# Optimization experiments

Measured on AMD Instinct MI355X. Metric: run time of the kernel, lower is better.

Reference implementation:

```python
import jax, jax.numpy as jnp
import numpy as np

TIME_PENALTY = 0.01
PONDER_EPS = 0.01
TIME_LIMIT = 16
BATCH, INPUT_SIZE, HIDDEN_SIZE = 4096, 1024, 1024


def setup_inputs() -> dict:
    key = jax.random.key(0)
    ks = jax.random.split(key, 8)
    s_in = 1.0 / np.sqrt(INPUT_SIZE + 1)
    s_h = 1.0 / np.sqrt(HIDDEN_SIZE)
    return {
        "inputs": jax.random.normal(ks[0], (BATCH, INPUT_SIZE), jnp.float32),
        "hidden": jax.random.normal(ks[1], (BATCH, HIDDEN_SIZE), jnp.float32),
        # RNNCell params (input size = INPUT_SIZE + 1 for the first-step flag)
        "W_ih": jax.random.uniform(ks[2], (HIDDEN_SIZE, INPUT_SIZE + 1), jnp.float32, -s_in, s_in),
        "b_ih": jax.random.uniform(ks[3], (HIDDEN_SIZE,), jnp.float32, -s_in, s_in),
        "W_hh": jax.random.uniform(ks[4], (HIDDEN_SIZE, HIDDEN_SIZE), jnp.float32, -s_h, s_h),
        "b_hh": jax.random.uniform(ks[5], (HIDDEN_SIZE,), jnp.float32, -s_h, s_h),
        # halting unit: Linear(hidden_size, 1), bias initialized to -1.0
        "W_halt": jax.random.uniform(ks[6], (1, HIDDEN_SIZE), jnp.float32, -s_h, s_h),
        "b_halt": jnp.full((1,), -1.0, jnp.float32),
    }


def _act_forward(inputs, hidden, W_ih, b_ih, W_hh, b_hh, W_halt, b_halt):
    B = inputs.shape[0]
    H = W_hh.shape[0]
    dt = inputs.dtype
    budget = jnp.asarray(1.0 - PONDER_EPS, dt)
    # input projection: the last input column is the first-step flag, so
    # step_inputs @ W_ih^T == inputs @ W_ih[:, :-1]^T + flag * W_ih[:, -1]
    x_base = inputs @ W_ih[:, :-1].T + b_ih  # (B, H)
    flag_col = W_ih[:, -1]                    # (H,)
    flags = (jnp.arange(TIME_LIMIT - 1) == 0).astype(dt)

    def step(carry, flag):
        h, halt_accum, cont, tot_h, tot_rem, tot_steps = carry
        h = jnp.tanh(x_base + flag * flag_col + h @ W_hh.T + b_hh)  # (B, H)
        step_halt = jax.nn.sigmoid(h @ W_halt.T + b_halt)           # (B, 1)
        masked_halt = jnp.where(cont, step_halt, 0.0)
        # halt accumulator is detached in the original (torch.no_grad)
        halt_accum = halt_accum + jax.lax.stop_gradient(masked_halt)
        ending = cont & (halt_accum + step_halt > budget)
        cont = cont & (~ending)
        tot_steps = tot_steps + cont.astype(dt)
        masked_rem = jnp.where(ending, 1.0 - halt_accum, 0.0)
        combined = masked_halt + masked_rem
        tot_h = tot_h + combined * h
        tot_rem = tot_rem + masked_halt
        return (h, halt_accum, cont, tot_h, tot_rem, tot_steps), None

    init = (
        hidden,
        jnp.zeros((B, 1), dt),
        jnp.ones((B, 1), bool),
        jnp.zeros((B, H), dt),
        jnp.zeros((B, 1), dt),
        jnp.zeros((B, 1), dt),
    )
    (h, halt_accum, cont, tot_h, tot_rem, tot_steps), _ = jax.lax.scan(step, init, flags)
    # for-else branch: elements still continuing after the loop get the remainder
    # (zero-contribution if everything halted early, matching the early break)
    tot_h = tot_h + jnp.where(cont, 1.0 - halt_accum, 0.0) * h
    ponder_cost = -TIME_PENALTY * tot_rem.mean()
    return tot_h, ponder_cost, tot_steps + 1.0


def reference(inputs, hidden, W_ih, b_ih, W_hh, b_hh, W_halt, b_halt):
    return _act_forward(inputs, hidden, W_ih, b_ih, W_hh, b_hh, W_halt, b_halt)
```

## Files before the change

kernel.cpp:

```cpp
#include <hip/hip_runtime.h>
#include <math.h>

#define BATCH 4096
#define HID   1024
#define KDIM  1024
#define NSTEP 15
#define KV    3072
#define NCHUNK (KV / 64)

#define TMM 128
#define TNN 64
#define LDAH 72

typedef _Float16 half8 __attribute__((ext_vector_type(8)));
typedef float floatx4 __attribute__((ext_vector_type(4)));

__device__ __forceinline__ _Float16 f16hi(float x) { return (_Float16)x; }

__global__ __launch_bounds__(256) void setup_kernel(
    const float* __restrict__ W_ih, const float* __restrict__ W_hh,
    const float* __restrict__ inputs, const float* __restrict__ hidden,
    _Float16* __restrict__ B3ih, _Float16* __restrict__ B3hh,
    _Float16* __restrict__ Ihi, _Float16* __restrict__ Ilo,
    _Float16* __restrict__ Hhi, _Float16* __restrict__ Hlo,
    float* __restrict__ flagcol, int* __restrict__ list0, int* __restrict__ counts,
    float* __restrict__ halt_accum, float* __restrict__ tot_rem) {
    size_t idx = (size_t)blockIdx.x * 256 + threadIdx.x;
    {
        float x = inputs[idx];
        _Float16 h = f16hi(x);
        Ihi[idx] = h; Ilo[idx] = (_Float16)(x - (float)h);
        float y = hidden[idx];
        _Float16 g = f16hi(y);
        Hhi[idx] = g; Hlo[idx] = (_Float16)(y - (float)g);
    }
    if (idx < (size_t)KDIM * KDIM) {
        int n = (int)(idx >> 10), k = (int)(idx & 1023);
        float w = W_hh[idx];
        _Float16 hi = f16hi(w);
        _Float16 lo = (_Float16)(w - (float)hi);
        size_t base = (size_t)n * KV;
        B3hh[base + k] = hi; B3hh[base + 1024 + k] = lo; B3hh[base + 2048 + k] = hi;
        float w2 = W_ih[(size_t)n * 1025 + k];
        _Float16 hi2 = f16hi(w2);
        _Float16 lo2 = (_Float16)(w2 - (float)hi2);
        B3ih[base + k] = hi2; B3ih[base + 1024 + k] = lo2; B3ih[base + 2048 + k] = hi2;
    }
    if (idx < BATCH) { list0[idx] = idx; halt_accum[idx] = 0.f; tot_rem[idx] = 0.f; }
    if (idx < KDIM) flagcol[idx] = W_ih[idx * 1025 + 1024];
    if (idx < 16) counts[idx] = (idx == 0) ? BATCH : 0;
}

__global__ __launch_bounds__(256) void mfma_step_kernel(
    const _Float16* __restrict__ Ahi, const _Float16* __restrict__ Alo,
    const _Float16* __restrict__ B3, const float* __restrict__ bias,
    const float* __restrict__ xbase, const float* __restrict__ flagcol, float flag,
    const int* __restrict__ list, const int* __restrict__ pcount,
    float* __restrict__ hout, _Float16* __restrict__ houthi, _Float16* __restrict__ houtlo,
    float* __restrict__ xout, int mode) {
    int count = pcount ? *pcount : BATCH;
    int row0 = blockIdx.x * TMM;
    if (row0 >= count) return;
    int col0 = blockIdx.y * TNN;

    __shared__ _Float16 Asm[2][TMM][LDAH];
    __shared__ _Float16 Bsm[2][TNN][LDAH];

    int t = threadIdx.x;
    int lane = t & 63, w = t >> 6;
    int wm = (w & 1) * 64, wn = (w >> 1) * 32;

    int arw[4], aq8[4]; size_t aoff[4];
#pragma unroll
    for (int l = 0; l < 4; l++) {
        int q = t + l * 256;
        int r = q >> 3, qk = q & 7;
        arw[l] = r; aq8[l] = qk * 8;
        int rr = row0 + r;
        int g = (rr < count) ? (list ? list[rr] : rr) : 0;
        aoff[l] = (size_t)g * KDIM + qk * 8;
    }
    int brw[2], bq8[2]; size_t boff[2];
#pragma unroll
    for (int l = 0; l < 2; l++) {
        int q = t + l * 256;
        int r = q >> 3, qk = q & 7;
        brw[l] = r; bq8[l] = qk * 8;
        boff[l] = (size_t)(col0 + r) * KV + qk * 8;
    }

    floatx4 acc[4][2];
#pragma unroll
    for (int i = 0; i < 4; i++)
#pragma unroll
        for (int j = 0; j < 2; j++) acc[i][j] = (floatx4)(0.f);

    int l15 = lane & 15, l4 = lane >> 4;

    half8 av[4], bv[2];
#pragma unroll
    for (int l = 0; l < 4; l++) av[l] = *(const half8*)(Ahi + aoff[l]);
#pragma unroll
    for (int l = 0; l < 2; l++) bv[l] = *(const half8*)(B3 + boff[l]);
#pragma unroll
    for (int l = 0; l < 4; l++) *(half8*)(&Asm[0][arw[l]][aq8[l]]) = av[l];
#pragma unroll
    for (int l = 0; l < 2; l++) *(half8*)(&Bsm[0][brw[l]][bq8[l]]) = bv[l];
    __syncthreads();

    int p = 0;
    for (int it = 0; it < NCHUNK; it++) {
        if (it + 1 < NCHUNK) {
            int k0v = (it + 1) << 6;
            const _Float16* Asrc = (k0v < 2048) ? Ahi : Alo;
            int kp = k0v & 1023;
#pragma unroll
            for (int l = 0; l < 4; l++) av[l] = *(const half8*)(Asrc + aoff[l] + kp);
#pragma unroll
            for (int l = 0; l < 2; l++) bv[l] = *(const half8*)(B3 + boff[l] + k0v);
        }
#pragma unroll
        for (int ks = 0; ks < 2; ks++) {
            int ko = ks * 32 + l4 * 8;
            half8 af[4], bf[2];
#pragma unroll
            for (int fi = 0; fi < 4; fi++)
                af[fi] = *(const half8*)(&Asm[p][wm + fi * 16 + l15][ko]);
#pragma unroll
            for (int fj = 0; fj < 2; fj++)
                bf[fj] = *(const half8*)(&Bsm[p][wn + fj * 16 + l15][ko]);
#pragma unroll
            for (int fi = 0; fi < 4; fi++)
#pragma unroll
                for (int fj = 0; fj < 2; fj++)
                    acc[fi][fj] = __builtin_amdgcn_mfma_f32_16x16x32_f16(
                        af[fi], bf[fj], acc[fi][fj], 0, 0, 0);
        }
        if (it + 1 < NCHUNK) {
            int q = p ^ 1;
#pragma unroll
            for (int l = 0; l < 4; l++) *(half8*)(&Asm[q][arw[l]][aq8[l]]) = av[l];
#pragma unroll
            for (int l = 0; l < 2; l++) *(half8*)(&Bsm[q][brw[l]][bq8[l]]) = bv[l];
        }
        __syncthreads();
        p ^= 1;
    }

#pragma unroll
    for (int fi = 0; fi < 4; fi++) {
#pragma unroll
        for (int rr = 0; rr < 4; rr++) {
            int lm = wm + fi * 16 + l4 * 4 + rr;
            int grd = row0 + lm;
            if (grd >= count) continue;
            int g = list ? list[grd] : grd;
#pragma unroll
            for (int fj = 0; fj < 2; fj++) {
                int c = col0 + wn + fj * 16 + l15;
                float v = acc[fi][fj][rr];
                if (mode == 0) {
                    xout[(size_t)g * KDIM + c] = v + bias[c];
                } else {
                    v += xbase[(size_t)g * KDIM + c] + flag * flagcol[c] + bias[c];
                    v = tanhf(v);
                    hout[(size_t)g * KDIM + c] = v;
                    _Float16 hi = f16hi(v);
                    houthi[(size_t)g * KDIM + c] = hi;
                    houtlo[(size_t)g * KDIM + c] = (_Float16)(v - (float)hi);
                }
            }
        }
    }
}

__global__ __launch_bounds__(256) void halt_kernel(
    const float* __restrict__ h, const float* __restrict__ W_halt,
    const float* __restrict__ b_halt,
    const int* __restrict__ list, const int* __restrict__ pcount,
    int* __restrict__ list_next, int* __restrict__ pcount_next,
    float* __restrict__ halt_accum, float* __restrict__ tot_rem,
    float* __restrict__ tot_h, float* __restrict__ steps_out,
    int stepnum, int first) {
    int count = *pcount;
    int wid = threadIdx.x >> 6, lane = threadIdx.x & 63;
    int r = blockIdx.x * 4 + wid;
    if (r >= count) return;
    int row = list[r];
    const float* hr = h + (size_t)row * HID;

    float dot = 0.f;
#pragma unroll
    for (int q = 0; q < 4; q++) {
        int c = q * 256 + lane * 4;
        float4 hv = *(const float4*)(hr + c);
        float4 wv = *(const float4*)(W_halt + c);
        dot += hv.x * wv.x + hv.y * wv.y + hv.z * wv.z + hv.w * wv.w;
    }
#pragma unroll
    for (int off = 32; off > 0; off >>= 1) dot += __shfl_down(dot, off);

    float combined = 0.f;
    if (lane == 0) {
        float p = 1.f / (1.f + expf(-(dot + b_halt[0])));
        float S = halt_accum[row] + p;
        halt_accum[row] = S;
        tot_rem[row] += p;
        bool ending = (S + p) > 0.99f;
        if (ending) {
            combined = p + (1.f - S);
            steps_out[row] = (float)stepnum;
        } else {
            combined = p;
            int idx = atomicAdd(pcount_next, 1);
            list_next[idx] = row;
        }
    }
    combined = __shfl(combined, 0);

    float* th = tot_h + (size_t)row * HID;
#pragma unroll
    for (int q = 0; q < 4; q++) {
        int c = q * 256 + lane * 4;
        float4 hv = *(const float4*)(hr + c);
        float4 ov;
        if (first) {
            ov.x = combined * hv.x; ov.y = combined * hv.y;
            ov.z = combined * hv.z; ov.w = combined * hv.w;
        } else {
            ov = *(const float4*)(th + c);
            ov.x += combined * hv.x; ov.y += combined * hv.y;
            ov.z += combined * hv.z; ov.w += combined * hv.w;
        }
        *(float4*)(th + c) = ov;
    }
}

__global__ __launch_bounds__(256) void epilogue_kernel(
    const float* __restrict__ h, const int* __restrict__ list,
    const int* __restrict__ pcount, const float* __restrict__ halt_accum,
    const float* __restrict__ tot_rem,
    float* __restrict__ tot_h, float* __restrict__ steps_out,
    float* __restrict__ ponder) {
    if (blockIdx.x == 1024) {
        __shared__ float red[4];
        int t = threadIdx.x;
        float v = 0.f;
#pragma unroll
        for (int i = 0; i < 16; i++) v += tot_rem[t + i * 256];
#pragma unroll
        for (int off = 32; off > 0; off >>= 1) v += __shfl_down(v, off);
        int lane = t & 63, wid = t >> 6;
        if (lane == 0) red[wid] = v;
        __syncthreads();
        if (t == 0) ponder[0] = (red[0] + red[1] + red[2] + red[3]) * (-0.01f / 4096.f);
        return;
    }
    int count = *pcount;
    int wid = threadIdx.x >> 6, lane = threadIdx.x & 63;
    int r = blockIdx.x * 4 + wid;
    if (r >= count) return;
    int row = list[r];
    float cmb = 1.f - halt_accum[row];
    if (lane == 0) steps_out[row] = 16.f;
    const float* hr = h + (size_t)row * HID;
    float* th = tot_h + (size_t)row * HID;
#pragma unroll
    for (int q = 0; q < 4; q++) {
        int c = q * 256 + lane * 4;
        float4 hv = *(const float4*)(hr + c);
        float4 ov = *(const float4*)(th + c);
        ov.x += cmb * hv.x; ov.y += cmb * hv.y;
        ov.z += cmb * hv.z; ov.w += cmb * hv.w;
        *(float4*)(th + c) = ov;
    }
}

extern "C" void kernel_launch(void* const* d_in, const int* in_sizes, int n_in,
                              void* d_out, int out_size, void* d_ws, size_t ws_size,
                              hipStream_t stream) {
    const float* inputs = (const float*)d_in[0];
    const float* hidden = (const float*)d_in[1];
    const float* W_ih   = (const float*)d_in[2];
    const float* b_ih   = (const float*)d_in[3];
    const float* W_hh   = (const float*)d_in[4];
    const float* b_hh   = (const float*)d_in[5];
    const float* W_halt = (const float*)d_in[6];
    const float* b_halt = (const float*)d_in[7];
    float* out = (float*)d_out;

    float* ws = (float*)d_ws;
    const size_t NM = (size_t)BATCH * HID;
    float* xbase = ws;
    float* h     = xbase + NM;
    _Float16* B3ih = (_Float16*)(h + NM);
    _Float16* B3hh = B3ih + (size_t)HID * KV;
    _Float16* Ahi0 = B3hh + (size_t)HID * KV;
    _Float16* Alo0 = Ahi0 + NM;
    _Float16* Ahi1 = Alo0 + NM;
    _Float16* Alo1 = Ahi1 + NM;
    float* flagcol = (float*)(Alo1 + NM);
    float* halt_accum = flagcol + KDIM;
    float* tot_rem = halt_accum + BATCH;
    int* list0 = (int*)(tot_rem + BATCH);
    int* list1 = list0 + BATCH;
    int* counts = list1 + BATCH;

    _Float16* Ahi[2] = {Ahi0, Ahi1};
    _Float16* Alo[2] = {Alo0, Alo1};
    int* lists[2] = {list0, list1};

    float* tot_h = out;
    float* ponder = out + NM;
    float* steps_out = ponder + 1;

    setup_kernel<<<16384, 256, 0, stream>>>(W_ih, W_hh, inputs, hidden,
                                            B3ih, B3hh, Ahi1, Alo1, Ahi0, Alo0,
                                            flagcol, list0, counts, halt_accum, tot_rem);

    mfma_step_kernel<<<dim3(32, 16), 256, 0, stream>>>(
        Ahi1, Alo1, B3ih, b_ih, nullptr, nullptr, 0.f, nullptr, nullptr,
        nullptr, nullptr, nullptr, xbase, 0);

    for (int t = 0; t < NSTEP; t++) {
        mfma_step_kernel<<<dim3(32, 16), 256, 0, stream>>>(
            Ahi[t & 1], Alo[t & 1], B3hh, b_hh, xbase, flagcol,
            (t == 0) ? 1.f : 0.f, lists[t & 1], counts + t,
            h, Ahi[(t + 1) & 1], Alo[(t + 1) & 1], nullptr, 1);
        halt_kernel<<<1024, 256, 0, stream>>>(h, W_halt, b_halt,
                                              lists[t & 1], counts + t,
                                              lists[(t + 1) & 1], counts + t + 1,
                                              halt_accum, tot_rem, tot_h, steps_out,
                                              t + 1, (t == 0) ? 1 : 0);
    }
    epilogue_kernel<<<1025, 256, 0, stream>>>(h, lists[1], counts + 15,
                                              halt_accum, tot_rem, tot_h, steps_out, ponder);
}
```

Baseline: 736.6 us.

## Pre-swizzle weights into MFMA fragment layout and drop fp32 hidden buffer

```diff
diff --git a/kernel.cpp b/kernel.cpp
--- a/kernel.cpp
+++ b/kernel.cpp
@@ -7,15 +7,17 @@
 #define NSTEP 15
 #define KV    3072
 #define NCHUNK (KV / 64)
-
-#define TMM 128
-#define TNN 64
-#define LDAH 72
+#define NSEC  (KV / 16)
+#define NT    (HID / 32)
+
 
 typedef _Float16 half8 __attribute__((ext_vector_type(8)));
-typedef float floatx4 __attribute__((ext_vector_type(4)));
-
-__device__ __forceinline__ _Float16 f16hi(float x) { return (_Float16)x; }
+typedef float floatx16 __attribute__((ext_vector_type(16)));
+
+__device__ __forceinline__ size_t b3addr(int n, int kv) {
+    return ((size_t)((n >> 5) * NSEC + (kv >> 4))) * 512 +
+           (size_t)(((n & 31) + 32 * ((kv >> 3) & 1)) * 8 + (kv & 7));
+}
 
 __global__ __launch_bounds__(256) void setup_kernel(
     const float* __restrict__ W_ih, const float* __restrict__ W_hh,
@@ -28,84 +30,79 @@
     size_t idx = (size_t)blockIdx.x * 256 + threadIdx.x;
     {
         float x = inputs[idx];
-        _Float16 h = f16hi(x);
+        _Float16 h = (_Float16)x;
         Ihi[idx] = h; Ilo[idx] = (_Float16)(x - (float)h);
         float y = hidden[idx];
-        _Float16 g = f16hi(y);
+        _Float16 g = (_Float16)y;
         Hhi[idx] = g; Hlo[idx] = (_Float16)(y - (float)g);
     }
     if (idx < (size_t)KDIM * KDIM) {
         int n = (int)(idx >> 10), k = (int)(idx & 1023);
         float w = W_hh[idx];
-        _Float16 hi = f16hi(w);
+        _Float16 hi = (_Float16)w;
         _Float16 lo = (_Float16)(w - (float)hi);
-        size_t base = (size_t)n * KV;
-        B3hh[base + k] = hi; B3hh[base + 1024 + k] = lo; B3hh[base + 2048 + k] = hi;
+        B3hh[b3addr(n, k)] = hi;
+        B3hh[b3addr(n, 1024 + k)] = lo;
+        B3hh[b3addr(n, 2048 + k)] = hi;
         float w2 = W_ih[(size_t)n * 1025 + k];
-        _Float16 hi2 = f16hi(w2);
+        _Float16 hi2 = (_Float16)w2;
         _Float16 lo2 = (_Float16)(w2 - (float)hi2);
-        B3ih[base + k] = hi2; B3ih[base + 1024 + k] = lo2; B3ih[base + 2048 + k] = hi2;
+        B3ih[b3addr(n, k)] = hi2;
+        B3ih[b3addr(n, 1024 + k)] = lo2;
+        B3ih[b3addr(n, 2048 + k)] = hi2;
     }
     if (idx < BATCH) { list0[idx] = idx; halt_accum[idx] = 0.f; tot_rem[idx] = 0.f; }
     if (idx < KDIM) flagcol[idx] = W_ih[idx * 1025 + 1024];
     if (idx < 16) counts[idx] = (idx == 0) ? BATCH : 0;
 }
 
-__global__ __launch_bounds__(256) void mfma_step_kernel(
+__global__ __launch_bounds__(128) void mfma_step_kernel(
     const _Float16* __restrict__ Ahi, const _Float16* __restrict__ Alo,
-    const _Float16* __restrict__ B3, const float* __restrict__ bias,
+    const _Float16* __restrict__ B3f, const float* __restrict__ bias,
     const float* __restrict__ xbase, const float* __restrict__ flagcol, float flag,
     const int* __restrict__ list, const int* __restrict__ pcount,
-    float* __restrict__ hout, _Float16* __restrict__ houthi, _Float16* __restrict__ houtlo,
+    _Float16* __restrict__ houthi, _Float16* __restrict__ houtlo,
     float* __restrict__ xout, int mode) {
     int count = pcount ? *pcount : BATCH;
-    int row0 = blockIdx.x * TMM;
+    int row0 = blockIdx.x * 64;
     if (row0 >= count) return;
-    int col0 = blockIdx.y * TNN;
-
-    __shared__ _Float16 Asm[2][TMM][LDAH];
-    __shared__ _Float16 Bsm[2][TNN][LDAH];
+    int col0 = blockIdx.y * 128;
+
+    __shared__ _Float16 Asm[2][64 * 64];
 
     int t = threadIdx.x;
     int lane = t & 63, w = t >> 6;
-    int wm = (w & 1) * 64, wn = (w >> 1) * 32;
-
-    int arw[4], aq8[4]; size_t aoff[4];
+    int l31 = lane & 31, l5 = lane >> 5;
+
+    int asl[4]; size_t aoff[4];
 #pragma unroll
     for (int l = 0; l < 4; l++) {
-        int q = t + l * 256;
+        int q = t + l * 128;
         int r = q >> 3, qk = q & 7;
-        arw[l] = r; aq8[l] = qk * 8;
+        asl[l] = r * 64 + ((qk ^ (r & 7)) << 3);
         int rr = row0 + r;
         int g = (rr < count) ? (list ? list[rr] : rr) : 0;
-        aoff[l] = (size_t)g * KDIM + qk * 8;
-    }
-    int brw[2], bq8[2]; size_t boff[2];
-#pragma unroll
-    for (int l = 0; l < 2; l++) {
-        int q = t + l * 256;
-        int r = q >> 3, qk = q & 7;
-        brw[l] = r; bq8[l] = qk * 8;
-        boff[l] = (size_t)(col0 + r) * KV + qk * 8;
-    }
-
-    floatx4 acc[4][2];
-#pragma unroll
-    for (int i = 0; i < 4; i++)
-#pragma unroll
-        for (int j = 0; j < 2; j++) acc[i][j] = (floatx4)(0.f);
-
-    int l15 = lane & 15, l4 = lane >> 4;
-
-    half8 av[4], bv[2];
+        aoff[l] = (size_t)g * KDIM + (size_t)(qk << 3);
+    }
+
+    const half8* B8 = (const half8*)B3f;
+    int nt0 = (col0 >> 5) + w * 2;
+    const half8* Bp0 = B8 + (size_t)nt0 * NSEC * 64;
+    const half8* Bp1 = B8 + (size_t)(nt0 + 1) * NSEC * 64;
+
+    floatx16 acc[2][2];
+#pragma unroll
+    for (int i = 0; i < 2; i++)
+#pragma unroll
+        for (int j = 0; j < 2; j++)
+#pragma unroll
+            for (int r = 0; r < 16; r++) acc[i][j][r] = 0.f;
+
+    half8 av[4];
 #pragma unroll
     for (int l = 0; l < 4; l++) av[l] = *(const half8*)(Ahi + aoff[l]);
 #pragma unroll
-    for (int l = 0; l < 2; l++) bv[l] = *(const half8*)(B3 + boff[l]);
-#pragma unroll
-    for (int l = 0; l < 4; l++) *(half8*)(&Asm[0][arw[l]][aq8[l]]) = av[l];
-#pragma unroll
-    for (int l = 0; l < 2; l++) *(half8*)(&Bsm[0][brw[l]][bq8[l]]) = bv[l];
+    for (int l = 0; l < 4; l++) *(half8*)(&Asm[0][asl[l]]) = av[l];
     __syncthreads();
 
     int p = 0;
@@ -113,59 +110,51 @@
         if (it + 1 < NCHUNK) {
             int k0v = (it + 1) << 6;
             const _Float16* Asrc = (k0v < 2048) ? Ahi : Alo;
-            int kp = k0v & 1023;
+            size_t kp = (size_t)(k0v & 1023);
 #pragma unroll
             for (int l = 0; l < 4; l++) av[l] = *(const half8*)(Asrc + aoff[l] + kp);
-#pragma unroll
-            for (int l = 0; l < 2; l++) bv[l] = *(const half8*)(B3 + boff[l] + k0v);
-        }
-#pragma unroll
-        for (int ks = 0; ks < 2; ks++) {
-            int ko = ks * 32 + l4 * 8;
-            half8 af[4], bf[2];
-#pragma unroll
-            for (int fi = 0; fi < 4; fi++)
-                af[fi] = *(const half8*)(&Asm[p][wm + fi * 16 + l15][ko]);
-#pragma unroll
-            for (int fj = 0; fj < 2; fj++)
-                bf[fj] = *(const half8*)(&Bsm[p][wn + fj * 16 + l15][ko]);
-#pragma unroll
-            for (int fi = 0; fi < 4; fi++)
-#pragma unroll
-                for (int fj = 0; fj < 2; fj++)
-                    acc[fi][fj] = __builtin_amdgcn_mfma_f32_16x16x32_f16(
-                        af[fi], bf[fj], acc[fi][fj], 0, 0, 0);
+        }
+#pragma unroll
+        for (int s = 0; s < 4; s++) {
+            int sg = it * 4 + s;
+            int gl = s * 2 + l5;
+            int ga = (gl ^ (l31 & 7)) << 3;
+            half8 a0 = *(const half8*)(&Asm[p][l31 * 64 + ga]);
+            half8 a1 = *(const half8*)(&Asm[p][(32 + l31) * 64 + ga]);
+            half8 b0 = Bp0[(size_t)sg * 64 + lane];
+            half8 b1 = Bp1[(size_t)sg * 64 + lane];
+            acc[0][0] = __builtin_amdgcn_mfma_f32_32x32x16_f16(a0, b0, acc[0][0], 0, 0, 0);
+            acc[0][1] = __builtin_amdgcn_mfma_f32_32x32x16_f16(a0, b1, acc[0][1], 0, 0, 0);
+            acc[1][0] = __builtin_amdgcn_mfma_f32_32x32x16_f16(a1, b0, acc[1][0], 0, 0, 0);
+            acc[1][1] = __builtin_amdgcn_mfma_f32_32x32x16_f16(a1, b1, acc[1][1], 0, 0, 0);
         }
         if (it + 1 < NCHUNK) {
             int q = p ^ 1;
 #pragma unroll
-            for (int l = 0; l < 4; l++) *(half8*)(&Asm[q][arw[l]][aq8[l]]) = av[l];
-#pragma unroll
-            for (int l = 0; l < 2; l++) *(half8*)(&Bsm[q][brw[l]][bq8[l]]) = bv[l];
+            for (int l = 0; l < 4; l++) *(half8*)(&Asm[q][asl[l]]) = av[l];
         }
         __syncthreads();
         p ^= 1;
     }
 
 #pragma unroll
-    for (int fi = 0; fi < 4; fi++) {
-#pragma unroll
-        for (int rr = 0; rr < 4; rr++) {
-            int lm = wm + fi * 16 + l4 * 4 + rr;
-            int grd = row0 + lm;
+    for (int fi = 0; fi < 2; fi++) {
+#pragma unroll
+        for (int r = 0; r < 16; r++) {
+            int rowid = (r & 3) + 8 * (r >> 2) + 4 * l5;
+            int grd = row0 + fi * 32 + rowid;
             if (grd >= count) continue;
             int g = list ? list[grd] : grd;
 #pragma unroll
             for (int fj = 0; fj < 2; fj++) {
-                int c = col0 + wn + fj * 16 + l15;
-                float v = acc[fi][fj][rr];
+                int c = col0 + w * 64 + fj * 32 + l31;
+                float v = acc[fi][fj][r];
                 if (mode == 0) {
                     xout[(size_t)g * KDIM + c] = v + bias[c];
                 } else {
                     v += xbase[(size_t)g * KDIM + c] + flag * flagcol[c] + bias[c];
                     v = tanhf(v);
-                    hout[(size_t)g * KDIM + c] = v;
-                    _Float16 hi = f16hi(v);
+                    _Float16 hi = (_Float16)v;
                     houthi[(size_t)g * KDIM + c] = hi;
                     houtlo[(size_t)g * KDIM + c] = (_Float16)(v - (float)hi);
                 }
@@ -175,8 +164,8 @@
 }
 
 __global__ __launch_bounds__(256) void halt_kernel(
-    const float* __restrict__ h, const float* __restrict__ W_halt,
-    const float* __restrict__ b_halt,
+    const _Float16* __restrict__ Hhi, const _Float16* __restrict__ Hlo,
+    const float* __restrict__ W_halt, const float* __restrict__ b_halt,
     const int* __restrict__ list, const int* __restrict__ pcount,
     int* __restrict__ list_next, int* __restrict__ pcount_next,
     float* __restrict__ halt_accum, float* __restrict__ tot_rem,
@@ -187,15 +176,22 @@
     int r = blockIdx.x * 4 + wid;
     if (r >= count) return;
     int row = list[r];
-    const float* hr = h + (size_t)row * HID;
-
+    const _Float16* hh = Hhi + (size_t)row * HID;
+    const _Float16* hl = Hlo + (size_t)row * HID;
+
+    float hv[16];
     float dot = 0.f;
 #pragma unroll
-    for (int q = 0; q < 4; q++) {
-        int c = q * 256 + lane * 4;
-        float4 hv = *(const float4*)(hr + c);
-        float4 wv = *(const float4*)(W_halt + c);
-        dot += hv.x * wv.x + hv.y * wv.y + hv.z * wv.z + hv.w * wv.w;
+    for (int q = 0; q < 2; q++) {
+        int c = q * 512 + lane * 8;
+        half8 h8 = *(const half8*)(hh + c);
+        half8 l8 = *(const half8*)(hl + c);
+#pragma unroll
+        for (int j = 0; j < 8; j++) {
+            float v = (float)h8[j] + (float)l8[j];
+            hv[q * 8 + j] = v;
+            dot += v * W_halt[c + j];
+        }
     }
 #pragma unroll
     for (int off = 32; off > 0; off >>= 1) dot += __shfl_down(dot, off);
@@ -220,26 +216,29 @@
 
     float* th = tot_h + (size_t)row * HID;
 #pragma unroll
-    for (int q = 0; q < 4; q++) {
-        int c = q * 256 + lane * 4;
-        float4 hv = *(const float4*)(hr + c);
-        float4 ov;
-        if (first) {
-            ov.x = combined * hv.x; ov.y = combined * hv.y;
-            ov.z = combined * hv.z; ov.w = combined * hv.w;
-        } else {
-            ov = *(const float4*)(th + c);
-            ov.x += combined * hv.x; ov.y += combined * hv.y;
-            ov.z += combined * hv.z; ov.w += combined * hv.w;
-        }
-        *(float4*)(th + c) = ov;
+    for (int q = 0; q < 2; q++) {
+        int c = q * 512 + lane * 8;
+#pragma unroll
+        for (int j = 0; j < 8; j += 4) {
+            float4 ov;
+            if (first) {
+                ov = make_float4(0.f, 0.f, 0.f, 0.f);
+            } else {
+                ov = *(const float4*)(th + c + j);
+            }
+            ov.x += combined * hv[q * 8 + j + 0];
+            ov.y += combined * hv[q * 8 + j + 1];
+            ov.z += combined * hv[q * 8 + j + 2];
+            ov.w += combined * hv[q * 8 + j + 3];
+            *(float4*)(th + c + j) = ov;
+        }
     }
 }
 
 __global__ __launch_bounds__(256) void epilogue_kernel(
-    const float* __restrict__ h, const int* __restrict__ list,
-    const int* __restrict__ pcount, const float* __restrict__ halt_accum,
-    const float* __restrict__ tot_rem,
+    const _Float16* __restrict__ Hhi, const _Float16* __restrict__ Hlo,
+    const int* __restrict__ list, const int* __restrict__ pcount,
+    const float* __restrict__ halt_accum, const float* __restrict__ tot_rem,
     float* __restrict__ tot_h, float* __restrict__ steps_out,
     float* __restrict__ ponder) {
     if (blockIdx.x == 1024) {
@@ -263,16 +262,23 @@
     int row = list[r];
     float cmb = 1.f - halt_accum[row];
     if (lane == 0) steps_out[row] = 16.f;
-    const float* hr = h + (size_t)row * HID;
+    const _Float16* hh = Hhi + (size_t)row * HID;
+    const _Float16* hl = Hlo + (size_t)row * HID;
     float* th = tot_h + (size_t)row * HID;
 #pragma unroll
-    for (int q = 0; q < 4; q++) {
-        int c = q * 256 + lane * 4;
-        float4 hv = *(const float4*)(hr + c);
-        float4 ov = *(const float4*)(th + c);
-        ov.x += cmb * hv.x; ov.y += cmb * hv.y;
-        ov.z += cmb * hv.z; ov.w += cmb * hv.w;
-        *(float4*)(th + c) = ov;
+    for (int q = 0; q < 2; q++) {
+        int c = q * 512 + lane * 8;
+        half8 h8 = *(const half8*)(hh + c);
+        half8 l8 = *(const half8*)(hl + c);
+#pragma unroll
+        for (int j = 0; j < 8; j += 4) {
+            float4 ov = *(const float4*)(th + c + j);
+            ov.x += cmb * ((float)h8[j + 0] + (float)l8[j + 0]);
+            ov.y += cmb * ((float)h8[j + 1] + (float)l8[j + 1]);
+            ov.z += cmb * ((float)h8[j + 2] + (float)l8[j + 2]);
+            ov.w += cmb * ((float)h8[j + 3] + (float)l8[j + 3]);
+            *(float4*)(th + c + j) = ov;
+        }
     }
 }
 
@@ -292,8 +298,7 @@
     float* ws = (float*)d_ws;
     const size_t NM = (size_t)BATCH * HID;
     float* xbase = ws;
-    float* h     = xbase + NM;
-    _Float16* B3ih = (_Float16*)(h + NM);
+    _Float16* B3ih = (_Float16*)(xbase + NM);
     _Float16* B3hh = B3ih + (size_t)HID * KV;
     _Float16* Ahi0 = B3hh + (size_t)HID * KV;
     _Float16* Alo0 = Ahi0 + NM;
@@ -318,21 +323,22 @@
                                             B3ih, B3hh, Ahi1, Alo1, Ahi0, Alo0,
                                             flagcol, list0, counts, halt_accum, tot_rem);
 
-    mfma_step_kernel<<<dim3(32, 16), 256, 0, stream>>>(
+    mfma_step_kernel<<<dim3(64, 8), 128, 0, stream>>>(
         Ahi1, Alo1, B3ih, b_ih, nullptr, nullptr, 0.f, nullptr, nullptr,
-        nullptr, nullptr, nullptr, xbase, 0);
+        nullptr, nullptr, xbase, 0);
 
     for (int t = 0; t < NSTEP; t++) {
-        mfma_step_kernel<<<dim3(32, 16), 256, 0, stream>>>(
+        mfma_step_kernel<<<dim3(64, 8), 128, 0, stream>>>(
             Ahi[t & 1], Alo[t & 1], B3hh, b_hh, xbase, flagcol,
             (t == 0) ? 1.f : 0.f, lists[t & 1], counts + t,
-            h, Ahi[(t + 1) & 1], Alo[(t + 1) & 1], nullptr, 1);
-        halt_kernel<<<1024, 256, 0, stream>>>(h, W_halt, b_halt,
+            Ahi[(t + 1) & 1], Alo[(t + 1) & 1], nullptr, 1);
+        halt_kernel<<<1024, 256, 0, stream>>>(Ahi[(t + 1) & 1], Alo[(t + 1) & 1],
+                                              W_halt, b_halt,
                                               lists[t & 1], counts + t,
                                               lists[(t + 1) & 1], counts + t + 1,
                                               halt_accum, tot_rem, tot_h, steps_out,
                                               t + 1, (t == 0) ? 1 : 0);
     }
-    epilogue_kernel<<<1025, 256, 0, stream>>>(h, lists[1], counts + 15,
+    epilogue_kernel<<<1025, 256, 0, stream>>>(Ahi[0], Alo[0], lists[1], counts + 15,
                                               halt_accum, tot_rem, tot_h, steps_out, ponder);
 }
```

Result: slower. 1.098 ms (+49.0%).
